# Kernel tuning notes

Hardware: AMD Instinct MI355X
Metric: run time of the kernel (lower is better)

The kernel has to match this reference:

```python
import jax, jax.numpy as jnp
import numpy as np

B, LM, LX, D = 16, 1024, 1024, 768


def setup_inputs() -> dict:
    key = jax.random.key(0)
    k1, k2, k3, k4 = jax.random.split(key, 4)
    main = jax.random.normal(k1, (B, LM, D), dtype=jnp.float32)
    x = jax.random.normal(k2, (B, LX, D), dtype=jnp.float32)
    # keras 'uniform' init ~ U(-0.05, 0.05); scale to keep activations sane
    W = jax.random.uniform(k3, (D, D), dtype=jnp.float32, minval=-0.05, maxval=0.05)
    w = jax.random.uniform(k4, (2 * D, 1), dtype=jnp.float32, minval=-0.05, maxval=0.05)
    return {"main": main, "x": x, "W": W, "w": w}


def reference(main, x, W, w):
    # bilinear co-attention scores: (main @ W) . x^T -> (B, LM, LX)
    proj = jnp.einsum('bmd,de->bme', main, W)            # (B, LM, D)
    scores = jnp.einsum('bme,bne->bmn', proj, x)         # (B, LM, LX) -- no softmax in original
    A = jnp.einsum('bmn,bnd->bmd', scores, x)            # attended features (B, LM, D)
    s = main - A
    m = main * A
    outputs = jnp.concatenate([s, m], axis=-1)           # (B, LM, 2D)
    beta = jnp.einsum('bmk,k->bm', outputs, w[:, 0])     # (B, LM) -- raw, no softmax
    pooled = jnp.einsum('bm,bmk->bk', beta, outputs)     # weighted-sum pooling (B, 2D)
    return pooled
```

## Files before the change

kernel.cpp:

```cpp
#include <hip/hip_runtime.h>

constexpr int kB  = 16;
constexpr int kLM = 1024;
constexpr int kLX = 1024;
constexpr int kD  = 768;

using short8 = __attribute__((ext_vector_type(8))) short;
using f32x4  = __attribute__((ext_vector_type(4))) float;

__device__ __forceinline__ unsigned short f2bf(float f) {
    unsigned u = __float_as_uint(f);
    u = (u + 0x7FFF + ((u >> 16) & 1)) >> 16;
    return (unsigned short)u;
}
__device__ __forceinline__ float bf2f(unsigned short h) {
    return __uint_as_float(((unsigned)h) << 16);
}

__device__ __forceinline__ void gl_lds16(const unsigned short* g, unsigned short* l) {
    auto gp = (const __attribute__((address_space(1))) unsigned int*)g;
    auto lp = (__attribute__((address_space(3))) unsigned int*)l;
    __builtin_amdgcn_global_load_lds(gp, lp, 16, 0, 0);
}

__device__ __forceinline__ void writeChunk(unsigned short* dst, float4 lo, float4 hi) {
    union { short8 v; unsigned short u[8]; } o;
    o.u[0] = f2bf(lo.x); o.u[1] = f2bf(lo.y); o.u[2] = f2bf(lo.z); o.u[3] = f2bf(lo.w);
    o.u[4] = f2bf(hi.x); o.u[5] = f2bf(hi.y); o.u[6] = f2bf(hi.z); o.u[7] = f2bf(hi.w);
    *(short8*)dst = o.v;
}

__device__ __forceinline__ void gemm_core(
    const unsigned short* __restrict__ Ab, const unsigned short* __restrict__ Bb,
    unsigned short* __restrict__ Cb, unsigned short* __restrict__ Cm,
    int N, int K, unsigned short* As0, unsigned short* Bs0) {
    const int t    = threadIdx.x;
    const int wave = t >> 6, lane = t & 63;
    const int wr = (wave >> 1) * 64, wc = (wave & 1) * 64;
    const int quad = lane >> 4, l15 = lane & 15;

    size_t goff[4];
    int    lof[4];
#pragma unroll
    for (int m = 0; m < 4; ++m) {
        const int p   = t + 256 * m;
        const int row = p >> 3;
        const int ch  = (p & 7) ^ (row & 7);
        goff[m] = (size_t)row * K + ch * 8;
        lof[m]  = p * 8;
    }

    const int perm0 = quad ^ (l15 & 7);
    const int aOff  = (wr + l15) * 64 + perm0 * 8;
    const int bOff  = (wc + l15) * 64 + perm0 * 8;

    f32x4 acc[4][4];
    const f32x4 z = {0.f, 0.f, 0.f, 0.f};
#pragma unroll
    for (int i = 0; i < 4; ++i)
#pragma unroll
        for (int j = 0; j < 4; ++j) acc[i][j] = z;

    const int T = K >> 6;

    auto stage = [&](int kt, int sel) {
        const size_t k = (size_t)kt << 6;
        unsigned short* Ad = As0 + sel * 8192;
        unsigned short* Bd = Bs0 + sel * 8192;
#pragma unroll
        for (int m = 0; m < 4; ++m) gl_lds16(Ab + goff[m] + k, Ad + lof[m]);
#pragma unroll
        for (int m = 0; m < 4; ++m) gl_lds16(Bb + goff[m] + k, Bd + lof[m]);
    };

    stage(0, 0);
    stage(1, 1);

    for (int kt = 0; kt < T; ++kt) {
        if (kt + 1 < T) asm volatile("s_waitcnt vmcnt(8)" ::: "memory");
        else            asm volatile("s_waitcnt vmcnt(0)" ::: "memory");
        __builtin_amdgcn_s_barrier();
        asm volatile("" ::: "memory");

        const unsigned short* aP = As0 + (kt & 1) * 8192;
        const unsigned short* bP = Bs0 + (kt & 1) * 8192;
        short8 a0[4], b0[4], a1[4], b1[4];
#pragma unroll
        for (int i = 0; i < 4; ++i) a0[i] = *(const short8*)(aP + aOff + i * 1024);
#pragma unroll
        for (int j = 0; j < 4; ++j) b0[j] = *(const short8*)(bP + bOff + j * 1024);
        __builtin_amdgcn_s_setprio(1);
#pragma unroll
        for (int i = 0; i < 4; ++i)
#pragma unroll
            for (int j = 0; j < 4; ++j)
                acc[i][j] = __builtin_amdgcn_mfma_f32_16x16x32_bf16(
                    a0[i], b0[j], acc[i][j], 0, 0, 0);
        __builtin_amdgcn_s_setprio(0);
#pragma unroll
        for (int i = 0; i < 4; ++i) a1[i] = *(const short8*)(aP + (aOff ^ 32) + i * 1024);
#pragma unroll
        for (int j = 0; j < 4; ++j) b1[j] = *(const short8*)(bP + (bOff ^ 32) + j * 1024);
        __builtin_amdgcn_s_setprio(1);
#pragma unroll
        for (int i = 0; i < 4; ++i)
#pragma unroll
            for (int j = 0; j < 4; ++j)
                acc[i][j] = __builtin_amdgcn_mfma_f32_16x16x32_bf16(
                    a1[i], b1[j], acc[i][j], 0, 0, 0);
        __builtin_amdgcn_s_setprio(0);
        asm volatile("" ::: "memory");
        __builtin_amdgcn_s_barrier();
        if (kt + 2 < T) stage(kt + 2, kt & 1);
    }

    unsigned short* CbW = Cb + (size_t)wr * N + wc;
#pragma unroll
    for (int i = 0; i < 4; ++i)
#pragma unroll
        for (int j = 0; j < 4; ++j)
#pragma unroll
            for (int r = 0; r < 4; ++r)
                CbW[(size_t)(i * 16 + quad * 4 + r) * N + j * 16 + l15] =
                    f2bf(acc[i][j][r]);

    if (Cm) {
        unsigned short* CmW = Cm + (size_t)wc * N + wr;
#pragma unroll
        for (int i = 0; i < 4; ++i)
#pragma unroll
            for (int j = 0; j < 4; ++j) {
                ushort4 o;
                o.x = f2bf(acc[i][j][0]);
                o.y = f2bf(acc[i][j][1]);
                o.z = f2bf(acc[i][j][2]);
                o.w = f2bf(acc[i][j][3]);
                *(ushort4*)(CmW + (size_t)(j * 16 + l15) * N + i * 16 + quad * 4) = o;
            }
    }
}

__global__ __launch_bounds__(256) void prep_kernel(
    const float* __restrict__ x, unsigned short* __restrict__ xT,
    const float* __restrict__ W, unsigned short* __restrict__ WT,
    const float* __restrict__ mainp, unsigned short* __restrict__ mainBF) {
    const int bid = blockIdx.x;
    const int t   = threadIdx.x;
    if (bid < 3216) {
        __shared__ float tile[64][65];
        const float* src;
        unsigned short* dst;
        int ss, dstride;
        if (bid < 3072) {
            const int lb = bid & 15, rest = bid >> 4;
            const int db = rest % 12, b = rest / 12;
            src = x + ((size_t)b * kLX + lb * 64) * kD + db * 64;
            ss  = kD;
            dst = xT + ((size_t)b * kD + db * 64) * kLX + lb * 64;
            dstride = kLX;
        } else {
            const int ti = bid - 3072;
            const int d0 = (ti / 12) * 64, e0 = (ti % 12) * 64;
            src = W + (size_t)d0 * kD + e0;
            ss  = kD;
            dst = WT + (size_t)e0 * kD + d0;
            dstride = kD;
        }
        const int tx = t & 15, ty = t >> 4;
#pragma unroll
        for (int p = 0; p < 4; ++p) {
            int r = p * 16 + ty;
            float4 v = *(const float4*)(src + (size_t)r * ss + tx * 4);
            *(float4*)&tile[r][tx * 4] = v;
        }
        __syncthreads();
#pragma unroll
        for (int p = 0; p < 4; ++p) {
            int dr = p * 16 + ty;
            ushort4 o;
            o.x = f2bf(tile[tx * 4 + 0][dr]);
            o.y = f2bf(tile[tx * 4 + 1][dr]);
            o.z = f2bf(tile[tx * 4 + 2][dr]);
            o.w = f2bf(tile[tx * 4 + 3][dr]);
            *(ushort4*)(dst + (size_t)dr * dstride + tx * 4) = o;
        }
    } else {
        const long i = (long)(bid - 3216) * 256 + t;
        const long na8 = (long)kB * kLM * kD / 8;
        if (i >= na8) return;
        const float* s = mainp + i * 8;
        writeChunk(mainBF + i * 8, *(const float4*)s, *(const float4*)(s + 4));
    }
}

__global__ __launch_bounds__(256) void gemm_stage2_kernel(
    const unsigned short* __restrict__ xT,
    const unsigned short* __restrict__ mainBF,
    const unsigned short* __restrict__ WT,
    unsigned short* __restrict__ G, unsigned short* __restrict__ P) {
    __shared__ unsigned short As[2][8192];
    __shared__ unsigned short Bs[2][8192];
    const int wgid = blockIdx.x;
    const unsigned short *Ab, *Bb;
    unsigned short *Cb, *Cm = nullptr;
    int K;
    if (wgid < 336) {
        const int xcd = wgid & 7, kk = wgid >> 3;
        const int grp = kk / 21, til = kk - grp * 21;
        const int b   = grp * 8 + xcd;
        int bi = (int)((sqrtf(8.f * (float)til + 1.f) - 1.f) * 0.5f);
        if (bi * (bi + 1) / 2 > til) --bi;
        else if ((bi + 1) * (bi + 2) / 2 <= til) ++bi;
        const int bj = til - bi * (bi + 1) / 2;
        K = kLX;
        const unsigned short* base = xT + (size_t)b * kD * kLX;
        Ab = base + (size_t)bi * 128 * kLX;
        Bb = base + (size_t)bj * 128 * kLX;
        unsigned short* Gb = G + (size_t)b * kD * kD;
        Cb = Gb + (size_t)bi * 128 * kD + bj * 128;
        if (bi != bj) Cm = Gb + (size_t)bj * 128 * kD + bi * 128;
    } else {
        const int pid = wgid - 336;
        const int xcd = pid & 7, kk = pid >> 3;
        const int grp = kk / 48, til = kk - grp * 48;
        const int b   = grp * 8 + xcd;
        const int bi  = til & 7, bj = til >> 3;
        K = kD;
        Ab = mainBF + (size_t)b * kLM * kD + (size_t)bi * 128 * kD;
        Bb = WT + (size_t)bj * 128 * kD;
        Cb = P + (size_t)b * kLM * kD + (size_t)bi * 128 * kD + bj * 128;
    }
    gemm_core(Ab, Bb, Cb, Cm, kD, K, &As[0][0], &Bs[0][0]);
}

__global__ __launch_bounds__(256) void gemm_a_kernel(
    const unsigned short* __restrict__ P, const unsigned short* __restrict__ G,
    unsigned short* __restrict__ Ao) {
    __shared__ unsigned short As[2][8192];
    __shared__ unsigned short Bs[2][8192];
    const int wgid = blockIdx.x;
    const int xcd = wgid & 7, kk = wgid >> 3;
    const int grp = kk / 48, til = kk - grp * 48;
    const int b   = grp * 8 + xcd;
    const int bi  = til & 7, bj = til >> 3;
    const unsigned short* Ab = P + (size_t)b * kLM * kD + (size_t)bi * 128 * kD;
    const unsigned short* Bb = G + (size_t)b * kD * kD + (size_t)bj * 128 * kD;
    unsigned short* Cb = Ao + (size_t)b * kLM * kD + (size_t)bi * 128 * kD + bj * 128;
    gemm_core(Ab, Bb, Cb, nullptr, kD, kD, &As[0][0], &Bs[0][0]);
}

__global__ __launch_bounds__(256) void pool_kernel(
    const float* __restrict__ mainp, const unsigned short* __restrict__ Aout,
    const float* __restrict__ w, float* __restrict__ out) {
    __shared__ float red[4][24][64];
    const int b     = blockIdx.y;
    const int chunk = blockIdx.x;
    const int t     = threadIdx.x;
    const int wave  = t >> 6, lane = t & 63;
    float w1[12], w2[12], ps[12], pm[12];
#pragma unroll
    for (int s = 0; s < 12; ++s) {
        w1[s] = w[s * 64 + lane];
        w2[s] = w[kD + s * 64 + lane];
        ps[s] = 0.f; pm[s] = 0.f;
    }
#pragma unroll
    for (int rr = 0; rr < 4; ++rr) {
        const int row = chunk * 16 + rr * 4 + wave;
        const float* mr = mainp + ((size_t)b * kLM + row) * kD;
        const unsigned short* ar = Aout + ((size_t)b * kLM + row) * kD;
        float sv[12], mv[12], acc = 0.f;
#pragma unroll
        for (int s = 0; s < 12; ++s) {
            float m_ = mr[s * 64 + lane];
            float a_ = bf2f(ar[s * 64 + lane]);
            sv[s] = m_ - a_;
            mv[s] = m_ * a_;
            acc += sv[s] * w1[s] + mv[s] * w2[s];
        }
#pragma unroll
        for (int off = 32; off; off >>= 1) acc += __shfl_xor(acc, off);
#pragma unroll
        for (int s = 0; s < 12; ++s) { ps[s] += acc * sv[s]; pm[s] += acc * mv[s]; }
    }
#pragma unroll
    for (int s = 0; s < 12; ++s) {
        red[wave][s][lane]      = ps[s];
        red[wave][12 + s][lane] = pm[s];
    }
    __syncthreads();
    float* ob = out + (size_t)b * 2 * kD;
    for (int v = t; v < 24 * 64; v += 256) {
        const int sl = v >> 6, ln = v & 63;
        const float sum = red[0][sl][ln] + red[1][sl][ln] +
                          red[2][sl][ln] + red[3][sl][ln];
        const int d = (sl < 12) ? sl * 64 + ln : kD + (sl - 12) * 64 + ln;
        atomicAdd(&ob[d], sum);
    }
}

extern "C" void kernel_launch(void* const* d_in, const int* in_sizes, int n_in,
                              void* d_out, int out_size, void* d_ws, size_t ws_size,
                              hipStream_t stream) {
    const float* mainp = (const float*)d_in[0];
    const float* x     = (const float*)d_in[1];
    const float* W     = (const float*)d_in[2];
    const float* w     = (const float*)d_in[3];
    float* out = (float*)d_out;

    char* p = (char*)d_ws;
    unsigned short* xT     = (unsigned short*)p; p += (size_t)kB * kD * kLX * 2;
    unsigned short* G      = (unsigned short*)p; p += (size_t)kB * kD * kD * 2;
    unsigned short* P      = (unsigned short*)p; p += (size_t)kB * kLM * kD * 2;
    unsigned short* Ao     = (unsigned short*)p; p += (size_t)kB * kLM * kD * 2;
    unsigned short* WT     = (unsigned short*)p; p += (size_t)kD * kD * 2;
    unsigned short* mainBF = (unsigned short*)p; p += (size_t)kB * kLM * kD * 2;

    hipMemsetAsync(out, 0, (size_t)kB * 2 * kD * sizeof(float), stream);

    prep_kernel<<<dim3(3216 + kB * kLM * kD / 8 / 256), 256, 0, stream>>>(
        x, xT, W, WT, mainp, mainBF);

    gemm_stage2_kernel<<<dim3(336 + 768), 256, 0, stream>>>(xT, mainBF, WT, G, P);

    gemm_a_kernel<<<dim3(768), 256, 0, stream>>>(P, G, Ao);

    pool_kernel<<<dim3(kLM / 16, kB), 256, 0, stream>>>(mainp, Ao, w, out);
}
```

Baseline: 216.2 us.

## Use 256x256 GEMM tiles with 8 waves and phased in-loop prefetch

Replaces the 128x128, 4-wave GEMM core with a 256x256 tile computed by 8 waves, each owning 128x64 outputs. The global-to-LDS prefetch of the next K-slice is split into four pieces interleaved with four MFMA phases, using per-phase barriers. The larger tile raises arithmetic intensity and halves global traffic per FLOP. In exchange the grid shrinks to 288 and 192 workgroups, so the 256-CU part may be poorly filled with tail imbalance, and the extra barriers and register pressure could hurt.

```diff
diff --git a/kernel.cpp b/kernel.cpp
--- a/kernel.cpp
+++ b/kernel.cpp
@@ -30,93 +30,106 @@
     *(short8*)dst = o.v;
 }
 
-__device__ __forceinline__ void gemm_core(
+__device__ __forceinline__ void gemm_core256(
     const unsigned short* __restrict__ Ab, const unsigned short* __restrict__ Bb,
     unsigned short* __restrict__ Cb, unsigned short* __restrict__ Cm,
     int N, int K, unsigned short* As0, unsigned short* Bs0) {
     const int t    = threadIdx.x;
     const int wave = t >> 6, lane = t & 63;
-    const int wr = (wave >> 1) * 64, wc = (wave & 1) * 64;
+    const int wm = wave >> 2, wn = wave & 3;
     const int quad = lane >> 4, l15 = lane & 15;
 
     size_t goff[4];
     int    lof[4];
 #pragma unroll
     for (int m = 0; m < 4; ++m) {
-        const int p   = t + 256 * m;
+        const int p   = t + 512 * m;
         const int row = p >> 3;
         const int ch  = (p & 7) ^ (row & 7);
         goff[m] = (size_t)row * K + ch * 8;
         lof[m]  = p * 8;
     }
 
-    const int perm0 = quad ^ (l15 & 7);
-    const int aOff  = (wr + l15) * 64 + perm0 * 8;
-    const int bOff  = (wc + l15) * 64 + perm0 * 8;
-
-    f32x4 acc[4][4];
+    const int arow = wm * 128 + l15;
+    const int brow = wn * 64  + l15;
+    const int cx0  = quad ^ (l15 & 7);
+    const int cx1  = (4 + quad) ^ (l15 & 7);
+
+    f32x4 acc[8][4];
     const f32x4 z = {0.f, 0.f, 0.f, 0.f};
 #pragma unroll
-    for (int i = 0; i < 4; ++i)
+    for (int i = 0; i < 8; ++i)
 #pragma unroll
         for (int j = 0; j < 4; ++j) acc[i][j] = z;
 
     const int T = K >> 6;
 
-    auto stage = [&](int kt, int sel) {
-        const size_t k = (size_t)kt << 6;
-        unsigned short* Ad = As0 + sel * 8192;
-        unsigned short* Bd = Bs0 + sel * 8192;
-#pragma unroll
-        for (int m = 0; m < 4; ++m) gl_lds16(Ab + goff[m] + k, Ad + lof[m]);
-#pragma unroll
-        for (int m = 0; m < 4; ++m) gl_lds16(Bb + goff[m] + k, Bd + lof[m]);
+    auto stage = [&](const unsigned short* Gp, unsigned short* Ls, int kt, int h) {
+        const size_t kk = (size_t)kt << 6;
+        unsigned short* d = Ls + (kt & 1) * 16384;
+        gl_lds16(Gp + goff[2 * h]     + kk, d + lof[2 * h]);
+        gl_lds16(Gp + goff[2 * h + 1] + kk, d + lof[2 * h + 1]);
     };
 
-    stage(0, 0);
-    stage(1, 1);
+    stage(Ab, As0, 0, 0); stage(Ab, As0, 0, 1);
+    stage(Bb, Bs0, 0, 0); stage(Bb, Bs0, 0, 1);
 
     for (int kt = 0; kt < T; ++kt) {
-        if (kt + 1 < T) asm volatile("s_waitcnt vmcnt(8)" ::: "memory");
-        else            asm volatile("s_waitcnt vmcnt(0)" ::: "memory");
-        __builtin_amdgcn_s_barrier();
-        asm volatile("" ::: "memory");
-
-        const unsigned short* aP = As0 + (kt & 1) * 8192;
-        const unsigned short* bP = Bs0 + (kt & 1) * 8192;
-        short8 a0[4], b0[4], a1[4], b1[4];
-#pragma unroll
-        for (int i = 0; i < 4; ++i) a0[i] = *(const short8*)(aP + aOff + i * 1024);
-#pragma unroll
-        for (int j = 0; j < 4; ++j) b0[j] = *(const short8*)(bP + bOff + j * 1024);
-        __builtin_amdgcn_s_setprio(1);
-#pragma unroll
-        for (int i = 0; i < 4; ++i)
-#pragma unroll
-            for (int j = 0; j < 4; ++j)
-                acc[i][j] = __builtin_amdgcn_mfma_f32_16x16x32_bf16(
-                    a0[i], b0[j], acc[i][j], 0, 0, 0);
-        __builtin_amdgcn_s_setprio(0);
-#pragma unroll
-        for (int i = 0; i < 4; ++i) a1[i] = *(const short8*)(aP + (aOff ^ 32) + i * 1024);
-#pragma unroll
-        for (int j = 0; j < 4; ++j) b1[j] = *(const short8*)(bP + (bOff ^ 32) + j * 1024);
-        __builtin_amdgcn_s_setprio(1);
-#pragma unroll
-        for (int i = 0; i < 4; ++i)
-#pragma unroll
-            for (int j = 0; j < 4; ++j)
-                acc[i][j] = __builtin_amdgcn_mfma_f32_16x16x32_bf16(
-                    a1[i], b1[j], acc[i][j], 0, 0, 0);
-        __builtin_amdgcn_s_setprio(0);
-        asm volatile("" ::: "memory");
-        __builtin_amdgcn_s_barrier();
-        if (kt + 2 < T) stage(kt + 2, kt & 1);
-    }
-
-    unsigned short* CbW = Cb + (size_t)wr * N + wc;
-#pragma unroll
-    for (int i = 0; i < 4; ++i)
+        const unsigned short* aP = As0 + (kt & 1) * 16384;
+        const unsigned short* bP = Bs0 + (kt & 1) * 16384;
+        const bool pf = (kt + 1 < T);
+        short8 bg[4][2];
+#pragma unroll
+        for (int ph = 0; ph < 4; ++ph) {
+            short8 af[2][2];
+            if (ph == 0) {
+                if (pf) {
+                    stage(Ab, As0, kt + 1, 0);
+                    asm volatile("s_waitcnt vmcnt(2)" ::: "memory");
+                } else {
+                    asm volatile("s_waitcnt vmcnt(0)" ::: "memory");
+                }
+                __builtin_amdgcn_s_barrier();
+#pragma unroll
+                for (int nn = 0; nn < 4; ++nn) {
+                    const int ro = (brow + nn * 16) * 8;
+                    bg[nn][0] = *(const short8*)(bP + (ro + cx0) * 8);
+                    bg[nn][1] = *(const short8*)(bP + (ro + cx1) * 8);
+                }
+            }
+#pragma unroll
+            for (int mm = 0; mm < 2; ++mm) {
+                const int ro = (arow + (ph * 2 + mm) * 16) * 8;
+                af[mm][0] = *(const short8*)(aP + (ro + cx0) * 8);
+                af[mm][1] = *(const short8*)(aP + (ro + cx1) * 8);
+            }
+            if (pf) {
+                if (ph == 1)      stage(Ab, As0, kt + 1, 1);
+                else if (ph == 2) stage(Bb, Bs0, kt + 1, 0);
+                else if (ph == 3) stage(Bb, Bs0, kt + 1, 1);
+            }
+            if (ph != 0) __builtin_amdgcn_s_barrier();
+            asm volatile("s_waitcnt lgkmcnt(0)" ::: "memory");
+            __builtin_amdgcn_sched_barrier(0);
+            __builtin_amdgcn_s_setprio(1);
+#pragma unroll
+            for (int mm = 0; mm < 2; ++mm)
+#pragma unroll
+                for (int nn = 0; nn < 4; ++nn) {
+                    const int m = ph * 2 + mm;
+                    acc[m][nn] = __builtin_amdgcn_mfma_f32_16x16x32_bf16(
+                        af[mm][0], bg[nn][0], acc[m][nn], 0, 0, 0);
+                    acc[m][nn] = __builtin_amdgcn_mfma_f32_16x16x32_bf16(
+                        af[mm][1], bg[nn][1], acc[m][nn], 0, 0, 0);
+                }
+            __builtin_amdgcn_s_setprio(0);
+            __builtin_amdgcn_s_barrier();
+        }
+    }
+
+    unsigned short* CbW = Cb + (size_t)(wm * 128) * N + wn * 64;
+#pragma unroll
+    for (int i = 0; i < 8; ++i)
 #pragma unroll
         for (int j = 0; j < 4; ++j)
 #pragma unroll
@@ -125,9 +138,9 @@
                     f2bf(acc[i][j][r]);
 
     if (Cm) {
-        unsigned short* CmW = Cm + (size_t)wc * N + wr;
-#pragma unroll
-        for (int i = 0; i < 4; ++i)
+        unsigned short* CmW = Cm + (size_t)(wn * 64) * N + wm * 128;
+#pragma unroll
+        for (int i = 0; i < 8; ++i)
 #pragma unroll
             for (int j = 0; j < 4; ++j) {
                 ushort4 o;
@@ -193,60 +206,58 @@
     }
 }
 
-__global__ __launch_bounds__(256) void gemm_stage2_kernel(
+__global__ __launch_bounds__(512, 2) void gemm_stage2_kernel(
     const unsigned short* __restrict__ xT,
     const unsigned short* __restrict__ mainBF,
     const unsigned short* __restrict__ WT,
     unsigned short* __restrict__ G, unsigned short* __restrict__ P) {
-    __shared__ unsigned short As[2][8192];
-    __shared__ unsigned short Bs[2][8192];
+    __shared__ unsigned short As[2][16384];
+    __shared__ unsigned short Bs[2][16384];
     const int wgid = blockIdx.x;
     const unsigned short *Ab, *Bb;
     unsigned short *Cb, *Cm = nullptr;
     int K;
-    if (wgid < 336) {
+    if (wgid < 96) {
         const int xcd = wgid & 7, kk = wgid >> 3;
-        const int grp = kk / 21, til = kk - grp * 21;
+        const int grp = kk / 6, til = kk - grp * 6;
         const int b   = grp * 8 + xcd;
-        int bi = (int)((sqrtf(8.f * (float)til + 1.f) - 1.f) * 0.5f);
-        if (bi * (bi + 1) / 2 > til) --bi;
-        else if ((bi + 1) * (bi + 2) / 2 <= til) ++bi;
-        const int bj = til - bi * (bi + 1) / 2;
+        const int bi  = (til >= 3) ? 2 : ((til >= 1) ? 1 : 0);
+        const int bj  = til - bi * (bi + 1) / 2;
         K = kLX;
         const unsigned short* base = xT + (size_t)b * kD * kLX;
-        Ab = base + (size_t)bi * 128 * kLX;
-        Bb = base + (size_t)bj * 128 * kLX;
+        Ab = base + (size_t)bi * 256 * kLX;
+        Bb = base + (size_t)bj * 256 * kLX;
         unsigned short* Gb = G + (size_t)b * kD * kD;
-        Cb = Gb + (size_t)bi * 128 * kD + bj * 128;
-        if (bi != bj) Cm = Gb + (size_t)bj * 128 * kD + bi * 128;
+        Cb = Gb + (size_t)bi * 256 * kD + bj * 256;
+        if (bi != bj) Cm = Gb + (size_t)bj * 256 * kD + bi * 256;
     } else {
-        const int pid = wgid - 336;
+        const int pid = wgid - 96;
         const int xcd = pid & 7, kk = pid >> 3;
-        const int grp = kk / 48, til = kk - grp * 48;
+        const int grp = kk / 12, til = kk - grp * 12;
         const int b   = grp * 8 + xcd;
-        const int bi  = til & 7, bj = til >> 3;
+        const int bi  = til & 3, bj = til >> 2;
         K = kD;
-        Ab = mainBF + (size_t)b * kLM * kD + (size_t)bi * 128 * kD;
-        Bb = WT + (size_t)bj * 128 * kD;
-        Cb = P + (size_t)b * kLM * kD + (size_t)bi * 128 * kD + bj * 128;
-    }
-    gemm_core(Ab, Bb, Cb, Cm, kD, K, &As[0][0], &Bs[0][0]);
-}
-
-__global__ __launch_bounds__(256) void gemm_a_kernel(
+        Ab = mainBF + (size_t)b * kLM * kD + (size_t)bi * 256 * kD;
+        Bb = WT + (size_t)bj * 256 * kD;
+        Cb = P + (size_t)b * kLM * kD + (size_t)bi * 256 * kD + bj * 256;
+    }
+    gemm_core256(Ab, Bb, Cb, Cm, kD, K, &As[0][0], &Bs[0][0]);
+}
+
+__global__ __launch_bounds__(512, 2) void gemm_a_kernel(
     const unsigned short* __restrict__ P, const unsigned short* __restrict__ G,
     unsigned short* __restrict__ Ao) {
-    __shared__ unsigned short As[2][8192];
-    __shared__ unsigned short Bs[2][8192];
+    __shared__ unsigned short As[2][16384];
+    __shared__ unsigned short Bs[2][16384];
     const int wgid = blockIdx.x;
     const int xcd = wgid & 7, kk = wgid >> 3;
-    const int grp = kk / 48, til = kk - grp * 48;
+    const int grp = kk / 12, til = kk - grp * 12;
     const int b   = grp * 8 + xcd;
-    const int bi  = til & 7, bj = til >> 3;
-    const unsigned short* Ab = P + (size_t)b * kLM * kD + (size_t)bi * 128 * kD;
-    const unsigned short* Bb = G + (size_t)b * kD * kD + (size_t)bj * 128 * kD;
-    unsigned short* Cb = Ao + (size_t)b * kLM * kD + (size_t)bi * 128 * kD + bj * 128;
-    gemm_core(Ab, Bb, Cb, nullptr, kD, kD, &As[0][0], &Bs[0][0]);
+    const int bi  = til & 3, bj = til >> 2;
+    const unsigned short* Ab = P + (size_t)b * kLM * kD + (size_t)bi * 256 * kD;
+    const unsigned short* Bb = G + (size_t)b * kD * kD + (size_t)bj * 256 * kD;
+    unsigned short* Cb = Ao + (size_t)b * kLM * kD + (size_t)bi * 256 * kD + bj * 256;
+    gemm_core256(Ab, Bb, Cb, nullptr, kD, kD, &As[0][0], &Bs[0][0]);
 }
 
 __global__ __launch_bounds__(256) void pool_kernel(
@@ -321,9 +332,9 @@
     prep_kernel<<<dim3(3216 + kB * kLM * kD / 8 / 256), 256, 0, stream>>>(
         x, xT, W, WT, mainp, mainBF);
 
-    gemm_stage2_kernel<<<dim3(336 + 768), 256, 0, stream>>>(xT, mainBF, WT, G, P);
-
-    gemm_a_kernel<<<dim3(768), 256, 0, stream>>>(P, G, Ao);
+    gemm_stage2_kernel<<<dim3(288), 512, 0, stream>>>(xT, mainBF, WT, G, P);
+
+    gemm_a_kernel<<<dim3(192), 512, 0, stream>>>(P, G, Ao);
 
     pool_kernel<<<dim3(kLM / 16, kB), 256, 0, stream>>>(mainp, Ao, w, out);
 }
```

Result: slower. 236.2 us (+9.2%).

## Fuse fp32-to-bf16 conversion of main into GEMM loader and add persistent work queue

Applied to the files above, without the earlier changes.

Drops the separate pass that converts main to bf16 and writes it out. The P=main@W GEMM now loads fp32 main through registers, converts it and writes LDS directly, software-pipelined against the async B loads. The stage-2 GEMM also becomes a persistent kernel: 512 blocks pull tiles from per-XCD atomic counters, with the Gram tiles ordered first. This removes a full bf16 write and re-read of main, at the cost of a register-staged A path that is less asynchronous and an extra memset for the counters.

```diff
diff --git a/kernel.cpp b/kernel.cpp
--- a/kernel.cpp
+++ b/kernel.cpp
@@ -23,17 +23,21 @@
     __builtin_amdgcn_global_load_lds(gp, lp, 16, 0, 0);
 }
 
-__device__ __forceinline__ void writeChunk(unsigned short* dst, float4 lo, float4 hi) {
+__device__ __forceinline__ void writeChunkLDS(unsigned short* dst, float4 lo, float4 hi) {
     union { short8 v; unsigned short u[8]; } o;
     o.u[0] = f2bf(lo.x); o.u[1] = f2bf(lo.y); o.u[2] = f2bf(lo.z); o.u[3] = f2bf(lo.w);
     o.u[4] = f2bf(hi.x); o.u[5] = f2bf(hi.y); o.u[6] = f2bf(hi.z); o.u[7] = f2bf(hi.w);
-    *(short8*)dst = o.v;
-}
-
-__device__ __forceinline__ void gemm_core(
-    const unsigned short* __restrict__ Ab, const unsigned short* __restrict__ Bb,
+    auto lp = (__attribute__((address_space(3))) short8*)dst;
+    *lp = o.v;
+}
+
+template <bool AFP32>
+__device__ __forceinline__ void gemm_core64(
+    const void* __restrict__ Av, const unsigned short* __restrict__ Bb,
     unsigned short* __restrict__ Cb, unsigned short* __restrict__ Cm,
     int N, int K, unsigned short* As0, unsigned short* Bs0) {
+    const unsigned short* Ah = AFP32 ? nullptr : (const unsigned short*)Av;
+    const float*          Af = AFP32 ? (const float*)Av : nullptr;
     const int t    = threadIdx.x;
     const int wave = t >> 6, lane = t & 63;
     const int wr = (wave >> 1) * 64, wc = (wave & 1) * 64;
@@ -63,22 +67,60 @@
 
     const int T = K >> 6;
 
-    auto stage = [&](int kt, int sel) {
-        const size_t k = (size_t)kt << 6;
-        unsigned short* Ad = As0 + sel * 8192;
-        unsigned short* Bd = Bs0 + sel * 8192;
-#pragma unroll
-        for (int m = 0; m < 4; ++m) gl_lds16(Ab + goff[m] + k, Ad + lof[m]);
-#pragma unroll
-        for (int m = 0; m < 4; ++m) gl_lds16(Bb + goff[m] + k, Bd + lof[m]);
+    auto stageB = [&](int kt) {
+        const size_t kk = (size_t)kt << 6;
+        unsigned short* Bd = Bs0 + (kt & 1) * 8192;
+#pragma unroll
+        for (int m = 0; m < 4; ++m) gl_lds16(Bb + goff[m] + kk, Bd + lof[m]);
     };
-
-    stage(0, 0);
-    stage(1, 1);
+    auto stageA = [&](int kt) {
+        const size_t kk = (size_t)kt << 6;
+        unsigned short* Ad = As0 + (kt & 1) * 8192;
+#pragma unroll
+        for (int m = 0; m < 4; ++m) gl_lds16(Ah + goff[m] + kk, Ad + lof[m]);
+    };
+    float4 pa[4][2];
+    auto ldA = [&](int kt) {
+        const size_t kk = (size_t)kt << 6;
+#pragma unroll
+        for (int m = 0; m < 4; ++m) {
+            const float* s = Af + goff[m] + kk;
+            pa[m][0] = *(const float4*)s;
+            pa[m][1] = *(const float4*)(s + 4);
+        }
+    };
+    auto wrA = [&](int kt) {
+        unsigned short* Ad = As0 + (kt & 1) * 8192;
+#pragma unroll
+        for (int m = 0; m < 4; ++m) writeChunkLDS(Ad + lof[m], pa[m][0], pa[m][1]);
+    };
+
+    if constexpr (AFP32) {
+        ldA(0); wrA(0);
+        stageB(0);
+        asm volatile("" ::: "memory");
+        if (T > 1) {
+            ldA(1);
+            asm volatile("" ::: "memory");
+            stageB(1);
+        }
+    } else {
+        stageA(0); stageB(0);
+        if (T > 1) { stageA(1); stageB(1); }
+    }
 
     for (int kt = 0; kt < T; ++kt) {
-        if (kt + 1 < T) asm volatile("s_waitcnt vmcnt(8)" ::: "memory");
-        else            asm volatile("s_waitcnt vmcnt(0)" ::: "memory");
+        if constexpr (AFP32) {
+            if (kt == 0) {
+                if (T > 1) asm volatile("s_waitcnt vmcnt(12) lgkmcnt(0)" ::: "memory");
+                else       asm volatile("s_waitcnt vmcnt(0) lgkmcnt(0)" ::: "memory");
+            } else {
+                asm volatile("s_waitcnt lgkmcnt(0)" ::: "memory");
+            }
+        } else {
+            if (kt + 1 < T) asm volatile("s_waitcnt vmcnt(8)" ::: "memory");
+            else            asm volatile("s_waitcnt vmcnt(0)" ::: "memory");
+        }
         __builtin_amdgcn_s_barrier();
         asm volatile("" ::: "memory");
 
@@ -111,7 +153,20 @@
         __builtin_amdgcn_s_setprio(0);
         asm volatile("" ::: "memory");
         __builtin_amdgcn_s_barrier();
-        if (kt + 2 < T) stage(kt + 2, kt & 1);
+
+        if constexpr (AFP32) {
+            if (kt + 1 < T) {
+                asm volatile("s_waitcnt vmcnt(0)" ::: "memory");
+                wrA(kt + 1);
+                if (kt + 2 < T) {
+                    stageB(kt + 2);
+                    asm volatile("" ::: "memory");
+                    ldA(kt + 2);
+                }
+            }
+        } else {
+            if (kt + 2 < T) { stageA(kt + 2); stageB(kt + 2); }
+        }
     }
 
     unsigned short* CbW = Cb + (size_t)wr * N + wc;
@@ -142,95 +197,90 @@
 
 __global__ __launch_bounds__(256) void prep_kernel(
     const float* __restrict__ x, unsigned short* __restrict__ xT,
-    const float* __restrict__ W, unsigned short* __restrict__ WT,
-    const float* __restrict__ mainp, unsigned short* __restrict__ mainBF) {
+    const float* __restrict__ W, unsigned short* __restrict__ WT) {
+    __shared__ float tile[64][65];
     const int bid = blockIdx.x;
     const int t   = threadIdx.x;
-    if (bid < 3216) {
-        __shared__ float tile[64][65];
-        const float* src;
-        unsigned short* dst;
-        int ss, dstride;
-        if (bid < 3072) {
-            const int lb = bid & 15, rest = bid >> 4;
-            const int db = rest % 12, b = rest / 12;
-            src = x + ((size_t)b * kLX + lb * 64) * kD + db * 64;
-            ss  = kD;
-            dst = xT + ((size_t)b * kD + db * 64) * kLX + lb * 64;
-            dstride = kLX;
-        } else {
-            const int ti = bid - 3072;
-            const int d0 = (ti / 12) * 64, e0 = (ti % 12) * 64;
-            src = W + (size_t)d0 * kD + e0;
-            ss  = kD;
-            dst = WT + (size_t)e0 * kD + d0;
-            dstride = kD;
-        }
-        const int tx = t & 15, ty = t >> 4;
-#pragma unroll
-        for (int p = 0; p < 4; ++p) {
-            int r = p * 16 + ty;
-            float4 v = *(const float4*)(src + (size_t)r * ss + tx * 4);
-            *(float4*)&tile[r][tx * 4] = v;
-        }
-        __syncthreads();
-#pragma unroll
-        for (int p = 0; p < 4; ++p) {
-            int dr = p * 16 + ty;
-            ushort4 o;
-            o.x = f2bf(tile[tx * 4 + 0][dr]);
-            o.y = f2bf(tile[tx * 4 + 1][dr]);
-            o.z = f2bf(tile[tx * 4 + 2][dr]);
-            o.w = f2bf(tile[tx * 4 + 3][dr]);
-            *(ushort4*)(dst + (size_t)dr * dstride + tx * 4) = o;
-        }
+    const float* src;
+    unsigned short* dst;
+    int ss, dstride;
+    if (bid < 3072) {
+        const int lb = bid & 15, rest = bid >> 4;
+        const int db = rest % 12, b = rest / 12;
+        src = x + ((size_t)b * kLX + lb * 64) * kD + db * 64;
+        ss  = kD;
+        dst = xT + ((size_t)b * kD + db * 64) * kLX + lb * 64;
+        dstride = kLX;
     } else {
-        const long i = (long)(bid - 3216) * 256 + t;
-        const long na8 = (long)kB * kLM * kD / 8;
-        if (i >= na8) return;
-        const float* s = mainp + i * 8;
-        writeChunk(mainBF + i * 8, *(const float4*)s, *(const float4*)(s + 4));
+        const int ti = bid - 3072;
+        const int d0 = (ti / 12) * 64, e0 = (ti % 12) * 64;
+        src = W + (size_t)d0 * kD + e0;
+        ss  = kD;
+        dst = WT + (size_t)e0 * kD + d0;
+        dstride = kD;
+    }
+    const int tx = t & 15, ty = t >> 4;
+#pragma unroll
+    for (int p = 0; p < 4; ++p) {
+        int r = p * 16 + ty;
+        float4 v = *(const float4*)(src + (size_t)r * ss + tx * 4);
+        *(float4*)&tile[r][tx * 4] = v;
+    }
+    __syncthreads();
+#pragma unroll
+    for (int p = 0; p < 4; ++p) {
+        int dr = p * 16 + ty;
+        ushort4 o;
+        o.x = f2bf(tile[tx * 4 + 0][dr]);
+        o.y = f2bf(tile[tx * 4 + 1][dr]);
+        o.z = f2bf(tile[tx * 4 + 2][dr]);
+        o.w = f2bf(tile[tx * 4 + 3][dr]);
+        *(ushort4*)(dst + (size_t)dr * dstride + tx * 4) = o;
     }
 }
 
 __global__ __launch_bounds__(256) void gemm_stage2_kernel(
     const unsigned short* __restrict__ xT,
-    const unsigned short* __restrict__ mainBF,
+    const float* __restrict__ mainp,
     const unsigned short* __restrict__ WT,
-    unsigned short* __restrict__ G, unsigned short* __restrict__ P) {
+    unsigned short* __restrict__ G, unsigned short* __restrict__ P,
+    int* __restrict__ ctr) {
     __shared__ unsigned short As[2][8192];
     __shared__ unsigned short Bs[2][8192];
-    const int wgid = blockIdx.x;
-    const unsigned short *Ab, *Bb;
-    unsigned short *Cb, *Cm = nullptr;
-    int K;
-    if (wgid < 336) {
-        const int xcd = wgid & 7, kk = wgid >> 3;
-        const int grp = kk / 21, til = kk - grp * 21;
-        const int b   = grp * 8 + xcd;
-        int bi = (int)((sqrtf(8.f * (float)til + 1.f) - 1.f) * 0.5f);
-        if (bi * (bi + 1) / 2 > til) --bi;
-        else if ((bi + 1) * (bi + 2) / 2 <= til) ++bi;
-        const int bj = til - bi * (bi + 1) / 2;
-        K = kLX;
-        const unsigned short* base = xT + (size_t)b * kD * kLX;
-        Ab = base + (size_t)bi * 128 * kLX;
-        Bb = base + (size_t)bj * 128 * kLX;
-        unsigned short* Gb = G + (size_t)b * kD * kD;
-        Cb = Gb + (size_t)bi * 128 * kD + bj * 128;
-        if (bi != bj) Cm = Gb + (size_t)bj * 128 * kD + bi * 128;
-    } else {
-        const int pid = wgid - 336;
-        const int xcd = pid & 7, kk = pid >> 3;
-        const int grp = kk / 48, til = kk - grp * 48;
-        const int b   = grp * 8 + xcd;
-        const int bi  = til & 7, bj = til >> 3;
-        K = kD;
-        Ab = mainBF + (size_t)b * kLM * kD + (size_t)bi * 128 * kD;
-        Bb = WT + (size_t)bj * 128 * kD;
-        Cb = P + (size_t)b * kLM * kD + (size_t)bi * 128 * kD + bj * 128;
-    }
-    gemm_core(Ab, Bb, Cb, Cm, kD, K, &As[0][0], &Bs[0][0]);
+    __shared__ int s_my;
+    const int xcd = blockIdx.x & 7;
+    for (;;) {
+        if (threadIdx.x == 0) s_my = atomicAdd(&ctr[xcd], 1);
+        __syncthreads();
+        const int my = s_my;
+        if (my >= 138) return;
+        if (my < 42) {
+            const int bt = my / 21, til = my - bt * 21;
+            const int b  = bt * 8 + xcd;
+            int bi = (int)((sqrtf(8.f * (float)til + 1.f) - 1.f) * 0.5f);
+            if (bi * (bi + 1) / 2 > til) --bi;
+            else if ((bi + 1) * (bi + 2) / 2 <= til) ++bi;
+            const int bj = til - bi * (bi + 1) / 2;
+            const unsigned short* base = xT + (size_t)b * kD * kLX;
+            unsigned short* Gb = G + (size_t)b * kD * kD;
+            gemm_core64<false>(
+                base + (size_t)bi * 128 * kLX,
+                base + (size_t)bj * 128 * kLX,
+                Gb + (size_t)bi * 128 * kD + bj * 128,
+                (bi != bj) ? Gb + (size_t)bj * 128 * kD + bi * 128 : nullptr,
+                kD, kLX, &As[0][0], &Bs[0][0]);
+        } else {
+            const int pp = my - 42;
+            const int bt = pp / 48, til = pp - bt * 48;
+            const int b  = bt * 8 + xcd;
+            const int bi = til & 7, bj = til >> 3;
+            gemm_core64<true>(
+                mainp + (size_t)b * kLM * kD + (size_t)bi * 128 * kD,
+                WT + (size_t)bj * 128 * kD,
+                P + (size_t)b * kLM * kD + (size_t)bi * 128 * kD + bj * 128,
+                nullptr, kD, kD, &As[0][0], &Bs[0][0]);
+        }
+    }
 }
 
 __global__ __launch_bounds__(256) void gemm_a_kernel(
@@ -246,7 +296,7 @@
     const unsigned short* Ab = P + (size_t)b * kLM * kD + (size_t)bi * 128 * kD;
     const unsigned short* Bb = G + (size_t)b * kD * kD + (size_t)bj * 128 * kD;
     unsigned short* Cb = Ao + (size_t)b * kLM * kD + (size_t)bi * 128 * kD + bj * 128;
-    gemm_core(Ab, Bb, Cb, nullptr, kD, kD, &As[0][0], &Bs[0][0]);
+    gemm_core64<false>(Ab, Bb, Cb, nullptr, kD, kD, &As[0][0], &Bs[0][0]);
 }
 
 __global__ __launch_bounds__(256) void pool_kernel(
@@ -309,19 +359,19 @@
     float* out = (float*)d_out;
 
     char* p = (char*)d_ws;
-    unsigned short* xT     = (unsigned short*)p; p += (size_t)kB * kD * kLX * 2;
-    unsigned short* G      = (unsigned short*)p; p += (size_t)kB * kD * kD * 2;
-    unsigned short* P      = (unsigned short*)p; p += (size_t)kB * kLM * kD * 2;
-    unsigned short* Ao     = (unsigned short*)p; p += (size_t)kB * kLM * kD * 2;
-    unsigned short* WT     = (unsigned short*)p; p += (size_t)kD * kD * 2;
-    unsigned short* mainBF = (unsigned short*)p; p += (size_t)kB * kLM * kD * 2;
+    unsigned short* xT  = (unsigned short*)p; p += (size_t)kB * kD * kLX * 2;
+    unsigned short* G   = (unsigned short*)p; p += (size_t)kB * kD * kD * 2;
+    unsigned short* P   = (unsigned short*)p; p += (size_t)kB * kLM * kD * 2;
+    unsigned short* Ao  = (unsigned short*)p; p += (size_t)kB * kLM * kD * 2;
+    unsigned short* WT  = (unsigned short*)p; p += (size_t)kD * kD * 2;
+    int*            ctr = (int*)p;            p += 8 * sizeof(int);
 
     hipMemsetAsync(out, 0, (size_t)kB * 2 * kD * sizeof(float), stream);
-
-    prep_kernel<<<dim3(3216 + kB * kLM * kD / 8 / 256), 256, 0, stream>>>(
-        x, xT, W, WT, mainp, mainBF);
-
-    gemm_stage2_kernel<<<dim3(336 + 768), 256, 0, stream>>>(xT, mainBF, WT, G, P);
+    hipMemsetAsync(ctr, 0, 8 * sizeof(int), stream);
+
+    prep_kernel<<<dim3(3216), 256, 0, stream>>>(x, xT, W, WT);
+
+    gemm_stage2_kernel<<<dim3(512), 256, 0, stream>>>(xT, mainp, WT, G, P, ctr);
 
     gemm_a_kernel<<<dim3(768), 256, 0, stream>>>(P, G, Ao);
 
```

Measured after the change: 256.7 us. +18.7%, slower.
